# Optimization experiments

Hardware: AMD Instinct MI355X
Metric: run time of the kernel (lower is better)

## Reference

```python
import jax, jax.numpy as jnp
import numpy as np

D_MODEL = 1024
N_HEADS = 8
D_KEYS = 128
D_LLM = 4096


def setup_inputs() -> dict:
    key = jax.random.key(0)
    ks = jax.random.split(key, 12)
    B, L, S = 8, 1024, 1000
    dk = D_KEYS * N_HEADS  # 1024
    inp = {
        "target_embedding": jax.random.normal(ks[0], (B, L, D_MODEL), jnp.float32),
        "source_embedding": jax.random.normal(ks[1], (S, D_LLM), jnp.float32),
        "value_embedding": jax.random.normal(ks[2], (S, D_LLM), jnp.float32),
        # nn.Linear weights are [out_features, in_features]
        "Wq": jax.random.normal(ks[3], (dk, D_MODEL), jnp.float32) * 0.02,
        "bq": jnp.zeros((dk,), jnp.float32),
        "Wk": jax.random.normal(ks[4], (dk, D_LLM), jnp.float32) * 0.02,
        "bk": jnp.zeros((dk,), jnp.float32),
        "Wv": jax.random.normal(ks[5], (dk, D_LLM), jnp.float32) * 0.02,
        "bv": jnp.zeros((dk,), jnp.float32),
        "Wo": jax.random.normal(ks[6], (D_LLM, dk), jnp.float32) * 0.02,
        "bo": jnp.zeros((D_LLM,), jnp.float32),
    }
    return inp


def reference(target_embedding, source_embedding, value_embedding,
              Wq, bq, Wk, bk, Wv, bv, Wo, bo):
    B, L, _ = target_embedding.shape
    S, _ = source_embedding.shape
    H, E = N_HEADS, D_KEYS
    # projections (torch Linear: x @ W.T + b)
    q = (target_embedding @ Wq.T + bq).reshape(B, L, H, E)
    k = (source_embedding @ Wk.T + bk).reshape(S, H, E)
    v = (value_embedding @ Wv.T + bv).reshape(S, H, E)
    scale = 1.0 / np.sqrt(E).astype(np.float32)
    # cross-attention of B*L queries over S shared prototypes
    scores = jnp.einsum('blhe,she->bhls', q, k)  # [B,H,L,S]
    A = jax.nn.softmax(scale * scores, axis=-1)  # dropout is identity in eval
    out = jnp.einsum('bhls,she->blhe', A, v).reshape(B, L, H * E)
    return out @ Wo.T + bo  # [B, L, D_LLM]
```

## Files before the change

### kernel.cpp

```cpp
#include <hip/hip_runtime.h>
#include <hip/hip_bf16.h>


typedef __attribute__((ext_vector_type(8))) short short8;
typedef __attribute__((ext_vector_type(4))) short short4v;
typedef __attribute__((ext_vector_type(4))) float f32x4;
typedef __attribute__((ext_vector_type(4))) int int4v;

#define DEVINL static __device__ __forceinline__

DEVINL unsigned short f2bf(float f) {
  union { float f; unsigned u; } v; v.f = f;
  unsigned r = v.u + 0x7FFFu + ((v.u >> 16) & 1u);
  return (unsigned short)(r >> 16);
}

DEVINL f32x4 zero4() { f32x4 z; z[0] = 0.f; z[1] = 0.f; z[2] = 0.f; z[3] = 0.f; return z; }
DEVINL short8 zero8() { short8 z; z[0]=0; z[1]=0; z[2]=0; z[3]=0; z[4]=0; z[5]=0; z[6]=0; z[7]=0; return z; }

DEVINL void load_lds16(const unsigned short* g, unsigned short* l) {
  __builtin_amdgcn_global_load_lds(
      (const __attribute__((address_space(1))) void*)g,
      (__attribute__((address_space(3))) void*)l, 16, 0, 0);
}

__global__ __launch_bounds__(256)
void cvt3_bf16(const float* __restrict__ s0, unsigned short* __restrict__ d0, int n0,
               const float* __restrict__ s1, unsigned short* __restrict__ d1, int n1,
               const float* __restrict__ s2, unsigned short* __restrict__ d2, int n2)
{
  int idx = (blockIdx.x * 256 + threadIdx.x) * 8;
  const float* s; unsigned short* d; int rel = idx;
  if (rel < n0) { s = s0; d = d0; }
  else {
    rel -= n0;
    if (rel < n1) { s = s1; d = d1; }
    else { rel -= n1; if (rel >= n2) return; s = s2; d = d2; }
  }
  f32x4 x0 = *(const f32x4*)(s + rel);
  f32x4 x1 = *(const f32x4*)(s + rel + 4);
  short8 o;
#pragma unroll
  for (int j = 0; j < 4; j++) { o[j] = (short)f2bf(x0[j]); o[4 + j] = (short)f2bf(x1[j]); }
  *(short8*)(d + rel) = o;
}

__global__ __launch_bounds__(256)
void cvt_kv(const float* __restrict__ src, const float* __restrict__ val,
            const float* __restrict__ wk, const float* __restrict__ wv,
            unsigned short* __restrict__ Sb, unsigned short* __restrict__ Vb,
            unsigned short* __restrict__ Wkb, unsigned short* __restrict__ Wvb)
{
  const int seg = blockIdx.x >> 11;
  const int e = (((blockIdx.x & 2047) * 256) + threadIdx.x) * 8;
  const float* s;
  unsigned short* d;
  bool pad = false;
  if (seg == 0)      { s = src; d = Sb;  pad = (e >> 12) >= 1000; }
  else if (seg == 1) { s = val; d = Vb;  pad = (e >> 12) >= 1000; }
  else if (seg == 2) { s = wk;  d = Wkb; }
  else               { s = wv;  d = Wvb; }
  short8 o;
  if (pad) {
    o = zero8();
  } else {
    f32x4 x0 = *(const f32x4*)(s + e);
    f32x4 x1 = *(const f32x4*)(s + e + 4);
#pragma unroll
    for (int j = 0; j < 4; j++) { o[j] = (short)f2bf(x0[j]); o[4 + j] = (short)f2bf(x1[j]); }
  }
  *(short8*)(d + e) = o;
}

__global__ __launch_bounds__(512, 2)
void gemm256(const unsigned short* __restrict__ A,
             const unsigned short* __restrict__ B,
             const float* __restrict__ bias, float cscale,
             float* __restrict__ C, int M, int N, int K)
{
  __shared__ unsigned short lds[65536];
  const int tid = threadIdx.x;
  const int lane = tid & 63, w = tid >> 6;
  const int wr = w >> 2, wc = w & 3;
  const int l15 = lane & 15, l4 = lane >> 4;

  const int nwg = gridDim.x;
  const int q8 = nwg >> 3;
  const int swz = (blockIdx.x & 7) * q8 + (blockIdx.x >> 3);
  const int nbx = N >> 8;
  const int bx = swz % nbx, by = swz / nbx;
  const int m0 = by << 8, n0 = bx << 8;

  const unsigned short* gA[2];
  const unsigned short* gB[2];
#pragma unroll
  for (int i = 0; i < 2; i++) {
    const int c = i * 512 + tid;
    const int row = 2 * (c >> 3) + ((c >> 2) & 1);
    const int k4 = (c & 3) ^ ((c >> 3) & 3);
    gA[i] = A + (size_t)(m0 + row) * K + k4 * 8;
    gB[i] = B + (size_t)(n0 + row) * K + k4 * 8;
  }

  const int e = wr * 128 + l15;
  const int f = wc * 64 + l15;
  const unsigned cA0 = ((unsigned)(e >> 1) << 7) + ((e & 1) << 6) + ((l4 ^ ((e >> 1) & 3)) << 4);
  const unsigned cB0 = 16384u + ((unsigned)(f >> 1) << 7) + ((f & 1) << 6) + ((l4 ^ ((f >> 1) & 3)) << 4);
  const char* ldsc = (const char*)lds;

  f32x4 acc[8][4];
#pragma unroll
  for (int i = 0; i < 8; i++)
#pragma unroll
    for (int j = 0; j < 4; j++) acc[i][j] = zero4();

  const int NT = K >> 5;

#pragma unroll
  for (int pt = 0; pt < 3; pt++) {
    unsigned short* db = lds + pt * 16384;
#pragma unroll
    for (int i = 0; i < 2; i++) {
      load_lds16(gA[i] + pt * 32, db + (i * 512 + w * 64) * 8);
      load_lds16(gB[i] + pt * 32, db + ((i + 2) * 512 + w * 64) * 8);
    }
  }
  asm volatile("s_waitcnt vmcnt(8)" ::: "memory");
  __builtin_amdgcn_sched_barrier(0);
  __builtin_amdgcn_s_barrier();
  __builtin_amdgcn_sched_barrier(0);

  int bcur = 0, bstg = 3;
  for (int t = 0; t < NT; ++t) {
    if (t + 3 < NT) {
      unsigned short* db = lds + bstg * 16384;
      const int kt = (t + 3) * 32;
#pragma unroll
      for (int i = 0; i < 2; i++) {
        load_lds16(gA[i] + kt, db + (i * 512 + w * 64) * 8);
        load_lds16(gB[i] + kt, db + ((i + 2) * 512 + w * 64) * 8);
      }
    }
    const unsigned bufb = (unsigned)bcur * 32768u;
    const short8* pA = (const short8*)(ldsc + bufb + cA0);
    const short8* pB = (const short8*)(ldsc + bufb + cB0);
    short8 af[8], bfr[4];
#pragma unroll
    for (int mt = 0; mt < 8; mt++) af[mt] = pA[mt * 64];
#pragma unroll
    for (int nt = 0; nt < 4; nt++) bfr[nt] = pB[nt * 64];

    __builtin_amdgcn_s_setprio(1);
#pragma unroll
    for (int mt = 0; mt < 8; mt++)
#pragma unroll
      for (int nt = 0; nt < 4; nt++)
        acc[mt][nt] = __builtin_amdgcn_mfma_f32_16x16x32_bf16(af[mt], bfr[nt], acc[mt][nt], 0, 0, 0);
    __builtin_amdgcn_s_setprio(0);

    if (t + 1 < NT) {
      if (t + 3 < NT)      asm volatile("s_waitcnt vmcnt(8)" ::: "memory");
      else if (t + 2 < NT) asm volatile("s_waitcnt vmcnt(4)" ::: "memory");
      else                 asm volatile("s_waitcnt vmcnt(0)" ::: "memory");
      __builtin_amdgcn_sched_barrier(0);
      __builtin_amdgcn_s_barrier();
      __builtin_amdgcn_sched_barrier(0);
    }
    bcur = (bcur + 1) & 3;
    bstg = (bstg + 1) & 3;
  }

#pragma unroll
  for (int nt = 0; nt < 4; nt++) {
    const int col = n0 + wc * 64 + nt * 16 + l15;
    const float bvv = bias[col];
#pragma unroll
    for (int mt = 0; mt < 8; mt++) {
      const int row = m0 + wr * 128 + mt * 16 + l4 * 4;
#pragma unroll
      for (int j = 0; j < 4; j++)
        C[(size_t)(row + j) * N + col] = (acc[mt][nt][j] + bvv) * cscale;
    }
  }
}

template<bool C_BF16>
__global__ __launch_bounds__(256)
void gemm_bb(const unsigned short* __restrict__ A,
             const unsigned short* __restrict__ B,
             const float* __restrict__ bias, float cscale, void* __restrict__ C_,
             int M, int N, int K)
{
  __shared__ unsigned short As[4096];
  __shared__ unsigned short Bs[4096];
  const int t = threadIdx.x;
  const int lane = t & 63, w = t >> 6;
  const int wm = w >> 1, wn = w & 1;
  const int l15 = lane & 15, l4 = lane >> 4;
  const int m0 = blockIdx.y * 128, n0 = blockIdx.x * 128;

  const int srow = w * 32 + (lane >> 2);
  const int scol = (lane & 3) * 8;
  const unsigned short* Ap = A + (size_t)(m0 + srow) * K + scol;
  const unsigned short* Bp = B + (size_t)(n0 + srow) * K + scol;
  unsigned short* AsW = &As[w * 1024];
  unsigned short* BsW = &Bs[w * 1024];

  f32x4 acc[4][4];
#pragma unroll
  for (int i = 0; i < 4; i++)
#pragma unroll
    for (int j = 0; j < 4; j++) acc[i][j] = zero4();

  for (int k0 = 0; k0 < K; k0 += 32) {
    if (k0) __syncthreads();
    load_lds16(Ap + k0, AsW);
    load_lds16(Ap + k0 + (size_t)16 * K, AsW + 512);
    load_lds16(Bp + k0, BsW);
    load_lds16(Bp + k0 + (size_t)16 * K, BsW + 512);
    __syncthreads();

    short8 af[4], bf[4];
#pragma unroll
    for (int mt = 0; mt < 4; mt++)
      af[mt] = *(const short8*)&As[(wm * 64 + mt * 16 + l15) * 32 + l4 * 8];
#pragma unroll
    for (int nt = 0; nt < 4; nt++)
      bf[nt] = *(const short8*)&Bs[(wn * 64 + nt * 16 + l15) * 32 + l4 * 8];
#pragma unroll
    for (int mt = 0; mt < 4; mt++)
#pragma unroll
      for (int nt = 0; nt < 4; nt++)
        acc[mt][nt] = __builtin_amdgcn_mfma_f32_16x16x32_bf16(af[mt], bf[nt], acc[mt][nt], 0, 0, 0);
  }

#pragma unroll
  for (int nt = 0; nt < 4; nt++) {
    const int col = n0 + wn * 64 + nt * 16 + l15;
    const float bvv = bias[col];
#pragma unroll
    for (int mt = 0; mt < 4; mt++) {
#pragma unroll
      for (int j = 0; j < 4; j++) {
        const int row = m0 + wm * 64 + mt * 16 + l4 * 4 + j;
        const float val = (acc[mt][nt][j] + bvv) * cscale;
        if constexpr (C_BF16)
          ((unsigned short*)C_)[(size_t)row * N + col] = f2bf(val);
        else
          ((float*)C_)[(size_t)row * N + col] = val;
      }
    }
  }
}

__global__ __launch_bounds__(256)
void gemm_splitk_bb(const unsigned short* __restrict__ Sb,
                    const unsigned short* __restrict__ Vb,
                    const unsigned short* __restrict__ Wkb,
                    const unsigned short* __restrict__ Wvb,
                    float* __restrict__ Pt)
{
  __shared__ unsigned short As[4096];
  __shared__ unsigned short Bs[4096];
  const int t = threadIdx.x;
  const int lane = t & 63, w = t >> 6;
  const int wm = w >> 1, wn = w & 1;
  const int l15 = lane & 15, l4 = lane >> 4;
  const int m0 = blockIdx.y * 128, n0 = blockIdx.x * 128;
  const int split = blockIdx.z & 3;
  const int tensor = blockIdx.z >> 2;
  const unsigned short* A = tensor ? Vb : Sb;
  const unsigned short* B = tensor ? Wvb : Wkb;
  const int kb = split * 1024;

  const int srow = w * 32 + (lane >> 2);
  const int scol = (lane & 3) * 8;
  const unsigned short* Ap = A + (size_t)(m0 + srow) * 4096 + kb + scol;
  const unsigned short* Bp = B + (size_t)(n0 + srow) * 4096 + kb + scol;
  unsigned short* AsW = &As[w * 1024];
  unsigned short* BsW = &Bs[w * 1024];

  f32x4 acc[4][4];
#pragma unroll
  for (int i = 0; i < 4; i++)
#pragma unroll
    for (int j = 0; j < 4; j++) acc[i][j] = zero4();

  for (int k0 = 0; k0 < 1024; k0 += 32) {
    if (k0) __syncthreads();
    load_lds16(Ap + k0, AsW);
    load_lds16(Ap + k0 + (size_t)16 * 4096, AsW + 512);
    load_lds16(Bp + k0, BsW);
    load_lds16(Bp + k0 + (size_t)16 * 4096, BsW + 512);
    __syncthreads();

    short8 af[4], bf[4];
#pragma unroll
    for (int mt = 0; mt < 4; mt++)
      af[mt] = *(const short8*)&As[(wm * 64 + mt * 16 + l15) * 32 + l4 * 8];
#pragma unroll
    for (int nt = 0; nt < 4; nt++)
      bf[nt] = *(const short8*)&Bs[(wn * 64 + nt * 16 + l15) * 32 + l4 * 8];
#pragma unroll
    for (int mt = 0; mt < 4; mt++)
#pragma unroll
      for (int nt = 0; nt < 4; nt++)
        acc[mt][nt] = __builtin_amdgcn_mfma_f32_16x16x32_bf16(af[mt], bf[nt], acc[mt][nt], 0, 0, 0);
  }

  if (tensor == 0) {
    float* C = Pt + (size_t)split * 1048576;
#pragma unroll
    for (int nt = 0; nt < 4; nt++) {
      const int col = n0 + wn * 64 + nt * 16 + l15;
#pragma unroll
      for (int mt = 0; mt < 4; mt++) {
#pragma unroll
        for (int j = 0; j < 4; j++) {
          const int row = m0 + wm * 64 + mt * 16 + l4 * 4 + j;
          C[(size_t)row * 1024 + col] = acc[mt][nt][j];
        }
      }
    }
  } else {
    float* C = Pt + 4194304 + (size_t)split * 1048576;
#pragma unroll
    for (int nt = 0; nt < 4; nt++) {
      const int col = n0 + wn * 64 + nt * 16 + l15;
#pragma unroll
      for (int mt = 0; mt < 4; mt++) {
        const int row0 = m0 + wm * 64 + mt * 16 + l4 * 4;
        *(f32x4*)&C[(size_t)col * 1024 + row0] = acc[mt][nt];
      }
    }
  }
}

__global__ __launch_bounds__(256)
void reduce_kv2(const float* __restrict__ Pt, const float* __restrict__ bk,
                const float* __restrict__ bv, unsigned short* __restrict__ Kb,
                unsigned short* __restrict__ Vt)
{
  const int bid = blockIdx.x;
  const int t = threadIdx.x;
  if (bid < 1000) {
    const int v4 = bid * 256 + t;
    const float* base = Pt + (size_t)v4 * 4;
    f32x4 s = *(const f32x4*)(base);
#pragma unroll
    for (int sp = 1; sp < 4; sp++) {
      f32x4 p = *(const f32x4*)(base + (size_t)sp * 1048576);
      s[0] += p[0]; s[1] += p[1]; s[2] += p[2]; s[3] += p[3];
    }
    const int col0 = (v4 * 4) & 1023;
    f32x4 bb = *(const f32x4*)(bk + col0);
    short4v o;
#pragma unroll
    for (int j = 0; j < 4; j++) o[j] = (short)f2bf(s[j] + bb[j]);
    *(short4v*)(Kb + (size_t)v4 * 4) = o;
  } else {
    const int v4 = (bid - 1000) * 256 + t;
    const float* base = Pt + 4194304 + (size_t)v4 * 4;
    f32x4 s = *(const f32x4*)(base);
#pragma unroll
    for (int sp = 1; sp < 4; sp++) {
      f32x4 p = *(const f32x4*)(base + (size_t)sp * 1048576);
      s[0] += p[0]; s[1] += p[1]; s[2] += p[2]; s[3] += p[3];
    }
    const int n = (v4 * 4) >> 10;
    const float bb = bv[n];
    short4v o;
#pragma unroll
    for (int j = 0; j < 4; j++) o[j] = (short)f2bf(s[j] + bb);
    *(short4v*)(Vt + (size_t)v4 * 4) = o;
  }
}

template<bool A_BF16, bool C_BF16, bool C_T>
__global__ __launch_bounds__(256)
void gemm_bt(const void* __restrict__ A_, const float* __restrict__ B,
             const float* __restrict__ bias, float cscale, void* __restrict__ C_,
             int M, int N, int K)
{
  __shared__ unsigned short As[128][40];
  __shared__ unsigned short Bs[128][40];
  const int t = threadIdx.x;
  const int lane = t & 63, w = t >> 6;
  const int wm = w >> 1, wn = w & 1;
  const int l15 = lane & 15, l4 = lane >> 4;
  const int m0 = blockIdx.y * 128, n0 = blockIdx.x * 128;
  const int srow = t >> 1, scol = (t & 1) * 16;

  f32x4 acc[4][4];
#pragma unroll
  for (int i = 0; i < 4; i++)
#pragma unroll
    for (int j = 0; j < 4; j++) acc[i][j] = zero4();

  const int am = m0 + srow;
  const int bn = n0 + srow;

  for (int k0 = 0; k0 < K; k0 += 32) {
    short8 av0, av1, bv0, bv1;
    if constexpr (A_BF16) {
      const unsigned short* A = (const unsigned short*)A_;
      if (am < M) {
        const unsigned short* p = A + (size_t)am * K + k0 + scol;
        av0 = *(const short8*)p;
        av1 = *(const short8*)(p + 8);
      } else { av0 = zero8(); av1 = zero8(); }
    } else {
      const float* A = (const float*)A_;
      if (am < M) {
        const float* p = A + (size_t)am * K + k0 + scol;
        f32x4 x0 = *(const f32x4*)(p);
        f32x4 x1 = *(const f32x4*)(p + 4);
        f32x4 x2 = *(const f32x4*)(p + 8);
        f32x4 x3 = *(const f32x4*)(p + 12);
#pragma unroll
        for (int i = 0; i < 4; i++) {
          av0[i]     = (short)f2bf(x0[i]);
          av0[4 + i] = (short)f2bf(x1[i]);
          av1[i]     = (short)f2bf(x2[i]);
          av1[4 + i] = (short)f2bf(x3[i]);
        }
      } else { av0 = zero8(); av1 = zero8(); }
    }
    {
      const float* p = B + (size_t)bn * K + k0 + scol;
      f32x4 x0 = *(const f32x4*)(p);
      f32x4 x1 = *(const f32x4*)(p + 4);
      f32x4 x2 = *(const f32x4*)(p + 8);
      f32x4 x3 = *(const f32x4*)(p + 12);
#pragma unroll
      for (int i = 0; i < 4; i++) {
        bv0[i]     = (short)f2bf(x0[i]);
        bv0[4 + i] = (short)f2bf(x1[i]);
        bv1[i]     = (short)f2bf(x2[i]);
        bv1[4 + i] = (short)f2bf(x3[i]);
      }
    }
    __syncthreads();
    *(short8*)&As[srow][scol]     = av0;
    *(short8*)&As[srow][scol + 8] = av1;
    *(short8*)&Bs[srow][scol]     = bv0;
    *(short8*)&Bs[srow][scol + 8] = bv1;
    __syncthreads();

    short8 af[4], bf[4];
#pragma unroll
    for (int mt = 0; mt < 4; mt++)
      af[mt] = *(const short8*)&As[wm * 64 + mt * 16 + l15][l4 * 8];
#pragma unroll
    for (int nt = 0; nt < 4; nt++)
      bf[nt] = *(const short8*)&Bs[wn * 64 + nt * 16 + l15][l4 * 8];
#pragma unroll
    for (int mt = 0; mt < 4; mt++)
#pragma unroll
      for (int nt = 0; nt < 4; nt++)
        acc[mt][nt] = __builtin_amdgcn_mfma_f32_16x16x32_bf16(af[mt], bf[nt], acc[mt][nt], 0, 0, 0);
  }

#pragma unroll
  for (int nt = 0; nt < 4; nt++) {
    const int col = n0 + wn * 64 + nt * 16 + l15;
    const float bvv = bias[col];
#pragma unroll
    for (int mt = 0; mt < 4; mt++) {
#pragma unroll
      for (int j = 0; j < 4; j++) {
        const int row = m0 + wm * 64 + mt * 16 + l4 * 4 + j;
        if (row < M) {
          float val = (acc[mt][nt][j] + bvv) * cscale;
          if constexpr (C_T)
            ((unsigned short*)C_)[(size_t)col * 1024 + row] = f2bf(val);
          else if constexpr (C_BF16)
            ((unsigned short*)C_)[(size_t)row * N + col] = f2bf(val);
          else
            ((float*)C_)[(size_t)row * N + col] = val;
        }
      }
    }
  }
}

__global__ __launch_bounds__(256, 2)
void attn_fused4(const unsigned short* __restrict__ Q,
                 const unsigned short* __restrict__ Kb,
                 const unsigned short* __restrict__ Vt,
                 unsigned short* __restrict__ Ob)
{
  __shared__ unsigned short Ks[2][32][136];
  __shared__ unsigned short Vs[2][128][40];

  const int t = threadIdx.x;
  const int lane = t & 63, w = t >> 6;
  const int g = lane >> 4, q = lane & 15;
  const int qt = blockIdx.x & 7, bh = blockIdx.x >> 3;
  const int b = bh >> 3, h = bh & 7;
  const int qrow0 = b * 1024 + qt * 128 + w * 32;

  const unsigned short* Kh = Kb + h * 128;
  const unsigned short* Vh = Vt + (size_t)h * 128 * 1024;

  short8 qf[2][4];
#pragma unroll
  for (int qn = 0; qn < 2; qn++) {
    const unsigned short* qp = Q + (size_t)(qrow0 + qn * 16 + q) * 1024 + h * 128;
#pragma unroll
    for (int kk = 0; kk < 4; kk++)
      qf[qn][kk] = *(const short8*)(qp + kk * 32 + g * 8);
  }

  f32x4 o[2][8];
#pragma unroll
  for (int qn = 0; qn < 2; qn++)
#pragma unroll
    for (int et = 0; et < 8; et++) o[qn][et] = zero4();
  float m_s[2] = {-__builtin_inff(), -__builtin_inff()};
  float l_s[2] = {0.f, 0.f};

  const int krow = t >> 3, kcol = (t & 7) * 16;
  const int vrow = t >> 1, vcol = (t & 1) * 16;

  {
    const unsigned short* kp = Kh + (size_t)min(krow, 999) * 1024 + kcol;
    short8 ka0 = *(const short8*)kp, ka1 = *(const short8*)(kp + 8);
    const unsigned short* vp = Vh + (size_t)vrow * 1024 + vcol;
    short8 va0 = *(const short8*)vp, va1 = *(const short8*)(vp + 8);
    *(short8*)&Ks[0][krow][kcol]     = ka0;
    *(short8*)&Ks[0][krow][kcol + 8] = ka1;
    *(short8*)&Vs[0][vrow][vcol]     = va0;
    *(short8*)&Vs[0][vrow][vcol + 8] = va1;
  }
  __syncthreads();

  int cur = 0;
  for (int tile = 0; tile < 32; ++tile) {
    const int s0 = tile * 32;
    const bool last = (s0 == 992);

    const int s0n = last ? 992 : s0 + 32;
    const unsigned short* kp = Kh + (size_t)min(s0n + krow, 999) * 1024 + kcol;
    short8 ka0 = *(const short8*)kp, ka1 = *(const short8*)(kp + 8);
    const unsigned short* vp = Vh + (size_t)vrow * 1024 + s0n + vcol;
    short8 va0 = *(const short8*)vp, va1 = *(const short8*)(vp + 8);

    short8 kf[2][4];
#pragma unroll
    for (int sc = 0; sc < 2; sc++)
#pragma unroll
      for (int kk = 0; kk < 4; kk++)
        kf[sc][kk] = *(const short8*)&Ks[cur][sc * 16 + q][kk * 32 + g * 8];

    f32x4 st[2][2];
    __builtin_amdgcn_s_setprio(1);
#pragma unroll
    for (int qn = 0; qn < 2; qn++)
#pragma unroll
      for (int sc = 0; sc < 2; sc++) {
        st[qn][sc] = zero4();
#pragma unroll
        for (int kk = 0; kk < 4; kk++)
          st[qn][sc] = __builtin_amdgcn_mfma_f32_16x16x32_bf16(kf[sc][kk], qf[qn][kk], st[qn][sc], 0, 0, 0);
      }
    __builtin_amdgcn_s_setprio(0);

    short8 vf[8];
#pragma unroll
    for (int et = 0; et < 8; et++)
      vf[et] = *(const short8*)&Vs[cur][et * 16 + q][g * 8];

#pragma unroll
    for (int qn = 0; qn < 2; qn++) {
      float a[8];
#pragma unroll
      for (int sc = 0; sc < 2; sc++)
#pragma unroll
        for (int j = 0; j < 4; j++) {
          float v = st[qn][sc][j];
          if (last) {
            const int sl = s0 + sc * 16 + 4 * g + j;
            v = (sl < 1000) ? v : -__builtin_inff();
          }
          a[sc * 4 + j] = v;
        }
      float pmax = fmaxf(fmaxf(fmaxf(a[0], a[1]), fmaxf(a[2], a[3])),
                         fmaxf(fmaxf(a[4], a[5]), fmaxf(a[6], a[7])));
      pmax = fmaxf(pmax, __shfl_xor(pmax, 16));
      pmax = fmaxf(pmax, __shfl_xor(pmax, 32));
      if (!__all(pmax - m_s[qn] <= 11.54f)) {
        const float mn = fmaxf(m_s[qn], pmax);
        const float alpha = exp2f(m_s[qn] - mn);
        m_s[qn] = mn;
        l_s[qn] *= alpha;
#pragma unroll
        for (int et = 0; et < 8; et++)
#pragma unroll
          for (int j = 0; j < 4; j++) o[qn][et][j] *= alpha;
      }
      float e8[8];
#pragma unroll
      for (int k = 0; k < 8; k++) e8[k] = exp2f(a[k] - m_s[qn]);
      float rs = ((e8[0] + e8[1]) + (e8[2] + e8[3])) + ((e8[4] + e8[5]) + (e8[6] + e8[7]));
      rs += __shfl_xor(rs, 16);
      rs += __shfl_xor(rs, 32);
      l_s[qn] += rs;

      int D0, D1, D2, D3;
      asm("v_cvt_pk_bf16_f32 %0, %1, %2" : "=v"(D0) : "v"(e8[0]), "v"(e8[1]));
      asm("v_cvt_pk_bf16_f32 %0, %1, %2" : "=v"(D1) : "v"(e8[2]), "v"(e8[3]));
      asm("v_cvt_pk_bf16_f32 %0, %1, %2" : "=v"(D2) : "v"(e8[4]), "v"(e8[5]));
      asm("v_cvt_pk_bf16_f32 %0, %1, %2" : "=v"(D3) : "v"(e8[6]), "v"(e8[7]));
      const int sA = q + ((g & 1) << 5);
      const int sB = sA + 16;
      const int a0 = __shfl(D0, sA), a1 = __shfl(D1, sA);
      const int a2 = __shfl(D2, sA), a3 = __shfl(D3, sA);
      const int b0 = __shfl(D0, sB), b1 = __shfl(D1, sB);
      const int b2 = __shfl(D2, sB), b3 = __shfl(D3, sB);
      const bool hi = (g >= 2);
      int4v pi;
      pi[0] = hi ? a2 : a0;
      pi[1] = hi ? a3 : a1;
      pi[2] = hi ? b2 : b0;
      pi[3] = hi ? b3 : b1;
      const short8 pf = __builtin_bit_cast(short8, pi);

      __builtin_amdgcn_s_setprio(1);
#pragma unroll
      for (int et = 0; et < 8; et++)
        o[qn][et] = __builtin_amdgcn_mfma_f32_16x16x32_bf16(vf[et], pf, o[qn][et], 0, 0, 0);
      __builtin_amdgcn_s_setprio(0);
    }

    *(short8*)&Ks[cur ^ 1][krow][kcol]     = ka0;
    *(short8*)&Ks[cur ^ 1][krow][kcol + 8] = ka1;
    *(short8*)&Vs[cur ^ 1][vrow][vcol]     = va0;
    *(short8*)&Vs[cur ^ 1][vrow][vcol + 8] = va1;
    __syncthreads();
    cur ^= 1;
  }

#pragma unroll
  for (int qn = 0; qn < 2; qn++) {
    const float inv = 1.0f / l_s[qn];
    unsigned short* op = Ob + (size_t)(qrow0 + qn * 16 + q) * 1024 + h * 128;
#pragma unroll
    for (int et = 0; et < 8; et++) {
      short4v o4;
#pragma unroll
      for (int j = 0; j < 4; j++) o4[j] = (short)f2bf(o[qn][et][j] * inv);
      *(short4v*)(op + et * 16 + 4 * g) = o4;
    }
  }
}

extern "C" void kernel_launch(void* const* d_in, const int* in_sizes, int n_in,
                              void* d_out, int out_size, void* d_ws, size_t ws_size,
                              hipStream_t stream) {
  const float* target = (const float*)d_in[0];
  const float* source = (const float*)d_in[1];
  const float* value  = (const float*)d_in[2];
  const float* Wq = (const float*)d_in[3];
  const float* bq = (const float*)d_in[4];
  const float* Wk = (const float*)d_in[5];
  const float* bk = (const float*)d_in[6];
  const float* Wv = (const float*)d_in[7];
  const float* bv = (const float*)d_in[8];
  const float* Wo = (const float*)d_in[9];
  const float* bo = (const float*)d_in[10];
  float* out = (float*)d_out;

  const float SCALE = 0.12751743f;

  char* ws = (char*)d_ws;
  unsigned short* Sb  = (unsigned short*)(ws);
  unsigned short* Vb  = (unsigned short*)(ws + 8388608);
  unsigned short* Qb  = (unsigned short*)(ws);
  unsigned short* Kb  = (unsigned short*)(ws + 16777216);
  unsigned short* Vt  = (unsigned short*)(ws + 18825216);
  unsigned short* Tb  = (unsigned short*)(ws + 20922368);
  unsigned short* Ab  = (unsigned short*)(ws + 20922368);
  unsigned short* Wqb = (unsigned short*)(ws + 37699584);
  unsigned short* Wob = (unsigned short*)(ws + 39796736);
  float* Pt = (float*)d_out;
  unsigned short* Wkb = (unsigned short*)((char*)d_out + 33554432);
  unsigned short* Wvb = (unsigned short*)((char*)d_out + 41943040);
  const size_t WS_NEED = 48185344;

  dim3 blk(256);
  if (ws_size >= WS_NEED) {
    cvt3_bf16<<<dim3(6656), blk, 0, stream>>>(
        target, Tb, 8192 * 1024, Wq, Wqb, 1024 * 1024, Wo, Wob, 4096 * 1024);
    cvt_kv<<<dim3(8192), blk, 0, stream>>>(
        source, value, Wk, Wv, Sb, Vb, Wkb, Wvb);
    gemm_splitk_bb<<<dim3(8, 8, 8), blk, 0, stream>>>(Sb, Vb, Wkb, Wvb, Pt);
    reduce_kv2<<<dim3(2024), blk, 0, stream>>>(Pt, bk, bv, Kb, Vt);
    gemm_bb<true><<<dim3(8, 64), blk, 0, stream>>>(
        Tb, Wqb, bq, SCALE, (void*)Qb, 8192, 1024, 1024);
    attn_fused4<<<dim3(512), blk, 0, stream>>>(Qb, Kb, Vt, Ab);
    gemm256<<<dim3(512), dim3(512), 0, stream>>>(
        Ab, Wob, bo, 1.0f, out, 8192, 4096, 1024);
  } else {
    gemm_bt<false, true, false><<<dim3(8, 64), blk, 0, stream>>>(
        (const void*)target, Wq, bq, SCALE, (void*)Qb, 8192, 1024, 1024);
    gemm_bt<false, true, false><<<dim3(8, 8), blk, 0, stream>>>(
        (const void*)source, Wk, bk, 1.0f, (void*)Kb, 1000, 1024, 4096);
    gemm_bt<false, true, true><<<dim3(8, 8), blk, 0, stream>>>(
        (const void*)value, Wv, bv, 1.0f, (void*)Vt, 1000, 1024, 4096);
    attn_fused4<<<dim3(512), blk, 0, stream>>>(Qb, Kb, Vt, Ab);
    gemm_bt<true, false, false><<<dim3(32, 64), blk, 0, stream>>>(
        (const void*)Ab, Wo, bo, 1.0f, (void*)out, 8192, 4096, 1024);
  }
}
```

Baseline: 245.7 us.

## Switch GEMM pipeline to double-buffered K=64 stages with fewer barriers

The 256x256 bf16 GEMM pipeline moves from four K=32 LDS buffers with three stages of prefetch to two K=64 buffers with single-stage prefetch. Each stage now runs two K=32 MFMA sub-steps before one barrier, which halves the barriers and waitcnts per unit of K. The cost is a shallower prefetch, since only one stage is in flight and the loop waits for vmcnt(0), so more global-load latency may be exposed.

```diff
diff --git a/kernel.cpp b/kernel.cpp
--- a/kernel.cpp
+++ b/kernel.cpp
@@ -91,21 +91,22 @@
   const int bx = swz % nbx, by = swz / nbx;
   const int m0 = by << 8, n0 = bx << 8;
 
-  const unsigned short* gA[2];
-  const unsigned short* gB[2];
-#pragma unroll
-  for (int i = 0; i < 2; i++) {
-    const int c = i * 512 + tid;
+  const unsigned short* gA[4];
+  const unsigned short* gB[4];
+#pragma unroll
+  for (int i = 0; i < 4; i++) {
+    const int c = (i & 1) * 512 + tid;
     const int row = 2 * (c >> 3) + ((c >> 2) & 1);
-    const int k4 = (c & 3) ^ ((c >> 3) & 3);
-    gA[i] = A + (size_t)(m0 + row) * K + k4 * 8;
-    gB[i] = B + (size_t)(n0 + row) * K + k4 * 8;
+    const int kh = i >> 1;
+    const int col = kh * 32 + ((c & 3) ^ ((c >> 3) & 3)) * 8;
+    gA[i] = A + (size_t)(m0 + row) * K + col;
+    gB[i] = B + (size_t)(n0 + row) * K + col;
   }
 
   const int e = wr * 128 + l15;
   const int f = wc * 64 + l15;
   const unsigned cA0 = ((unsigned)(e >> 1) << 7) + ((e & 1) << 6) + ((l4 ^ ((e >> 1) & 3)) << 4);
-  const unsigned cB0 = 16384u + ((unsigned)(f >> 1) << 7) + ((f & 1) << 6) + ((l4 ^ ((f >> 1) & 3)) << 4);
+  const unsigned cB0 = 32768u + ((unsigned)(f >> 1) << 7) + ((f & 1) << 6) + ((l4 ^ ((f >> 1) & 3)) << 4);
   const char* ldsc = (const char*)lds;
 
   f32x4 acc[8][4];
@@ -114,60 +115,56 @@
 #pragma unroll
     for (int j = 0; j < 4; j++) acc[i][j] = zero4();
 
-  const int NT = K >> 5;
-
-#pragma unroll
-  for (int pt = 0; pt < 3; pt++) {
-    unsigned short* db = lds + pt * 16384;
-#pragma unroll
-    for (int i = 0; i < 2; i++) {
-      load_lds16(gA[i] + pt * 32, db + (i * 512 + w * 64) * 8);
-      load_lds16(gB[i] + pt * 32, db + ((i + 2) * 512 + w * 64) * 8);
-    }
-  }
-  asm volatile("s_waitcnt vmcnt(8)" ::: "memory");
+  const int NT = K >> 6;
+
+#pragma unroll
+  for (int i = 0; i < 4; i++) {
+    const int d8 = ((i >> 1) * 1024 + (i & 1) * 512 + w * 64) * 8;
+    load_lds16(gA[i], lds + d8);
+    load_lds16(gB[i], lds + 2048 * 8 + d8);
+  }
+  asm volatile("s_waitcnt vmcnt(0)" ::: "memory");
   __builtin_amdgcn_sched_barrier(0);
   __builtin_amdgcn_s_barrier();
   __builtin_amdgcn_sched_barrier(0);
 
-  int bcur = 0, bstg = 3;
+  int cur = 0;
   for (int t = 0; t < NT; ++t) {
-    if (t + 3 < NT) {
-      unsigned short* db = lds + bstg * 16384;
-      const int kt = (t + 3) * 32;
-#pragma unroll
-      for (int i = 0; i < 2; i++) {
-        load_lds16(gA[i] + kt, db + (i * 512 + w * 64) * 8);
-        load_lds16(gB[i] + kt, db + ((i + 2) * 512 + w * 64) * 8);
+    if (t + 1 < NT) {
+      unsigned short* db = lds + (cur ^ 1) * 32768;
+      const int kt = (t + 1) * 64;
+#pragma unroll
+      for (int i = 0; i < 4; i++) {
+        const int d8 = ((i >> 1) * 1024 + (i & 1) * 512 + w * 64) * 8;
+        load_lds16(gA[i] + kt, db + d8);
+        load_lds16(gB[i] + kt, db + 2048 * 8 + d8);
       }
     }
-    const unsigned bufb = (unsigned)bcur * 32768u;
-    const short8* pA = (const short8*)(ldsc + bufb + cA0);
-    const short8* pB = (const short8*)(ldsc + bufb + cB0);
-    short8 af[8], bfr[4];
-#pragma unroll
-    for (int mt = 0; mt < 8; mt++) af[mt] = pA[mt * 64];
-#pragma unroll
-    for (int nt = 0; nt < 4; nt++) bfr[nt] = pB[nt * 64];
-
-    __builtin_amdgcn_s_setprio(1);
-#pragma unroll
-    for (int mt = 0; mt < 8; mt++)
-#pragma unroll
-      for (int nt = 0; nt < 4; nt++)
-        acc[mt][nt] = __builtin_amdgcn_mfma_f32_16x16x32_bf16(af[mt], bfr[nt], acc[mt][nt], 0, 0, 0);
-    __builtin_amdgcn_s_setprio(0);
-
+    const unsigned bufb = (unsigned)cur * 65536u;
+#pragma unroll
+    for (int kk = 0; kk < 2; kk++) {
+      const short8* pA = (const short8*)(ldsc + bufb + kk * 16384u + cA0);
+      const short8* pB = (const short8*)(ldsc + bufb + kk * 16384u + cB0);
+      short8 af[8], bfr[4];
+#pragma unroll
+      for (int mt = 0; mt < 8; mt++) af[mt] = pA[mt * 64];
+#pragma unroll
+      for (int nt = 0; nt < 4; nt++) bfr[nt] = pB[nt * 64];
+      __builtin_amdgcn_s_setprio(1);
+#pragma unroll
+      for (int mt = 0; mt < 8; mt++)
+#pragma unroll
+        for (int nt = 0; nt < 4; nt++)
+          acc[mt][nt] = __builtin_amdgcn_mfma_f32_16x16x32_bf16(af[mt], bfr[nt], acc[mt][nt], 0, 0, 0);
+      __builtin_amdgcn_s_setprio(0);
+    }
     if (t + 1 < NT) {
-      if (t + 3 < NT)      asm volatile("s_waitcnt vmcnt(8)" ::: "memory");
-      else if (t + 2 < NT) asm volatile("s_waitcnt vmcnt(4)" ::: "memory");
-      else                 asm volatile("s_waitcnt vmcnt(0)" ::: "memory");
+      asm volatile("s_waitcnt vmcnt(0)" ::: "memory");
       __builtin_amdgcn_sched_barrier(0);
       __builtin_amdgcn_s_barrier();
       __builtin_amdgcn_sched_barrier(0);
     }
-    bcur = (bcur + 1) & 3;
-    bstg = (bstg + 1) & 3;
+    cur ^= 1;
   }
 
 #pragma unroll
```

Result: no change. 248.0 us (median of 5 runs) (+0.9%).
